# Kernel tuning notes

Measured on AMD Instinct MI355X. Metric: run time of the kernel, lower is better.

Reference implementation:

```python
import jax, jax.numpy as jnp
import numpy as np

DIM = 256
QK_DIM = 256
NUM_HEADS = 8
N_WIN = 7
TOPK = 4
SCALE = QK_DIM ** (-0.5)


def setup_inputs() -> dict:
    key = jax.random.key(0)
    k1, k2, k3 = jax.random.split(key, 3)
    N, D, H, W, C = 2, 8, 56, 56, DIM
    x = jax.random.normal(k1, (N, D, H, W, C), dtype=jnp.float32)
    # QKVLinear: Linear(dim, qk_dim + qk_dim + dim)
    Wqkv = jax.random.normal(k2, (C, 2 * QK_DIM + DIM), dtype=jnp.float32) * 0.02
    bqkv = jnp.zeros((2 * QK_DIM + DIM,), dtype=jnp.float32)
    Wo = jax.random.normal(k3, (DIM, DIM), dtype=jnp.float32) * 0.02
    bo = jnp.zeros((DIM,), dtype=jnp.float32)
    return {"x": x, "Wqkv": Wqkv, "bqkv": bqkv, "Wo": Wo, "bo": bo}


def reference(x, Wqkv, bqkv, Wo, bo):
    N, D, H, W, C = x.shape
    j = i = N_WIN
    h, w = H // j, W // i
    p2, w2 = j * i, h * w
    n = N * D
    m = NUM_HEADS
    ch = QK_DIM // m   # qk head dim
    cv = DIM // m      # v head dim

    # n t (j h) (i w) c -> n t (j i) h w c
    xw = x.reshape(N, D, j, h, i, w, C).transpose(0, 1, 2, 4, 3, 5, 6)
    xw = xw.reshape(N, D, p2, h, w, C)

    # QKVLinear then split into q / kv
    qkv = xw @ Wqkv + bqkv                       # (N,D,p2,h,w,2qk+dim)
    q = qkv[..., :QK_DIM]                        # (N,D,p2,h,w,qk)
    kv = qkv[..., QK_DIM:]                       # (N,D,p2,h,w,qk+dim)

    # inter-frame shift: frame t uses kv of frame t+1; last frame keeps its own
    kv = jnp.concatenate([kv[:, 1:], kv[:, -1:]], axis=1)

    q = q.reshape(n, p2, h, w, QK_DIM)
    kv = kv.reshape(n, p2, h, w, QK_DIM + DIM)
    q_pix = q.reshape(n, p2, w2, QK_DIM)
    kv_pix = kv.reshape(n, p2, w2, QK_DIM + DIM)  # identity kv_down

    # window-level routing (diff_routing=False -> detached)
    q_win = jax.lax.stop_gradient(q.mean(axis=(2, 3)))                  # (n,p2,qk)
    k_win = jax.lax.stop_gradient(kv[..., :QK_DIM].mean(axis=(2, 3)))   # (n,p2,qk)
    attn_logit = jnp.einsum('npc,nqc->npq', q_win * SCALE, k_win)       # (n,p2,p2)
    topk_logit, r_idx = jax.lax.top_k(attn_logit, TOPK)                 # (n,p2,topk)
    r_weight = jax.nn.softmax(topk_logit, axis=-1)  # computed, unused (mul_weight='none')

    # gather kv of routed windows: (n,p2,topk,w2,qk+dim)
    kv_sel = jax.vmap(lambda kvp, idx: kvp[idx])(kv_pix, r_idx)

    k_sel = kv_sel[..., :QK_DIM].reshape(n, p2, TOPK * w2, m, ch)
    v_sel = kv_sel[..., QK_DIM:].reshape(n, p2, TOPK * w2, m, cv)
    qh = q_pix.reshape(n, p2, w2, m, ch)

    attn = jnp.einsum('npqmc,npkmc->npmqk', qh * SCALE, k_sel)  # (n,p2,m,w2,topk*w2)
    attn = jax.nn.softmax(attn, axis=-1)
    out = jnp.einsum('npmqk,npkmc->npqmc', attn, v_sel).reshape(n, p2, w2, C)

    # (n j i) (h w) c -> N D (j h) (i w) c
    out = out.reshape(N, D, j, i, h, w, C).transpose(0, 1, 2, 4, 3, 5, 6)
    out = out.reshape(N, D, H, W, C)
    out = out @ Wo + bo
    return out
```

## Files before the change

### kernel.cpp

```cpp
#include <hip/hip_runtime.h>
#include <hip/hip_bf16.h>
#include <math.h>

#define QSC 0.09016844f

typedef __attribute__((ext_vector_type(8))) short bf16x8;
typedef __attribute__((ext_vector_type(4))) float f32x4;

__device__ __forceinline__ ushort f2bf(float f) {
    unsigned u = __float_as_uint(f);
    return (ushort)((u + 0x7FFFu + ((u >> 16) & 1u)) >> 16);
}

__device__ __forceinline__ unsigned pk2bf(float a, float b) {
    __hip_bfloat162 h = __float22bfloat162_rn(make_float2(a, b));
    return *(unsigned*)&h;
}

__device__ __forceinline__ void gl_lds16(const ushort* g, ushort* l) {
    __builtin_amdgcn_global_load_lds(
        (const __attribute__((address_space(1))) unsigned int*)g,
        (__attribute__((address_space(3))) unsigned int*)l, 16, 0, 0);
}

__device__ __forceinline__ int swz(int row) { return (row ^ (row >> 2)) & 3; }

__device__ __forceinline__ int token_to_xrow(int t) {
    int nd  = t / 3136;
    int r   = t % 3136;
    int p   = r >> 6;
    int pix = r & 63;
    int j = p / 7, i = p % 7;
    int hh = pix >> 3, ww = pix & 7;
    return nd * 3136 + (j * 8 + hh) * 56 + (i * 8 + ww);
}

__global__ __launch_bounds__(256) void k_prep(const float* __restrict__ x,
                                              const float* __restrict__ Wqkv,
                                              const float* __restrict__ Wo,
                                              ushort* __restrict__ xg,
                                              float* __restrict__ xmean,
                                              ushort* __restrict__ Wqkvt,
                                              ushort* __restrict__ Wot) {
    int b = blockIdx.x;
    int tid = threadIdx.x;
    if (b >= 784) {
        int bb = b - 784;
        if (bb < 768) Wqkvt[bb * 256 + tid] = f2bf(Wqkv[(size_t)tid * 768 + bb]);
        else { int n = bb - 768; Wot[n * 256 + tid] = f2bf(Wo[(size_t)tid * 256 + n]); }
        return;
    }
    int nd = b / 49, p = b % 49;
    int j = p / 7, i = p % 7;
    const float* xb = x + ((size_t)nd * 3136 + (j * 8) * 56 + i * 8) * 256 + tid;
    ushort* xo = xg + (size_t)b * 64 * 256 + tid;
    float s = 0.f;
#pragma unroll 2
    for (int hh = 0; hh < 8; ++hh)
#pragma unroll
        for (int ww = 0; ww < 8; ++ww) {
            float v = xb[(size_t)(hh * 56 + ww) * 256];
            s += v;
            xo[(size_t)(hh * 8 + ww) * 256] = f2bf(v);
        }
    xmean[(size_t)b * 256 + tid] = s * (1.f / 64.f);
}

__global__ __launch_bounds__(256) void k_winproj(const float* __restrict__ xmean,
                                                 const float* __restrict__ Wqkv,
                                                 const float* __restrict__ bqkv,
                                                 float* __restrict__ qwin,
                                                 float* __restrict__ kwin) {
    __shared__ float As[16 * 68];
    __shared__ float Bs[16 * 64];
    const int tid = threadIdx.x;
    const int m0 = blockIdx.y * 64;
    const int n0 = blockIdx.x * 64;

    const int ar = tid >> 2;
    const int ak = (tid & 3) * 4;
    const int arow = (m0 + ar < 784) ? (m0 + ar) : 783;
    const float* aptr = xmean + (size_t)arow * 256 + ak;

    const int bk = tid >> 4;
    const int bn = (tid & 15) * 4;
    const float* bptr = Wqkv + (size_t)bk * 768 + n0 + bn;

    const int ty = tid >> 4, tx = tid & 15;
    float acc[4][4] = {};

    for (int kt = 0; kt < 256; kt += 16) {
        float4 av = *(const float4*)(aptr + kt);
        float4 bv = *(const float4*)(bptr + (size_t)kt * 768);
        __syncthreads();
        As[(ak + 0) * 68 + ar] = av.x;
        As[(ak + 1) * 68 + ar] = av.y;
        As[(ak + 2) * 68 + ar] = av.z;
        As[(ak + 3) * 68 + ar] = av.w;
        *(float4*)&Bs[bk * 64 + bn] = bv;
        __syncthreads();
#pragma unroll
        for (int kk = 0; kk < 16; ++kk) {
            float4 a4 = *(const float4*)&As[kk * 68 + ty * 4];
            float4 b4 = *(const float4*)&Bs[kk * 64 + tx * 4];
            float a[4] = {a4.x, a4.y, a4.z, a4.w};
            float b[4] = {b4.x, b4.y, b4.z, b4.w};
#pragma unroll
            for (int ii = 0; ii < 4; ++ii)
#pragma unroll
                for (int jj = 0; jj < 4; ++jj) acc[ii][jj] += a[ii] * b[jj];
        }
    }
#pragma unroll
    for (int ii = 0; ii < 4; ++ii) {
        int t = m0 + ty * 4 + ii;
        if (t >= 784) continue;
#pragma unroll
        for (int jj = 0; jj < 4; ++jj) {
            int col = n0 + tx * 4 + jj;
            float v = acc[ii][jj] + bqkv[col];
            if (col < 256) qwin[(size_t)t * 256 + col] = v;
            else           kwin[(size_t)t * 256 + (col - 256)] = v;
        }
    }
}

__global__ __launch_bounds__(64) void k_route(const float* __restrict__ qwin,
                                              const float* __restrict__ kwin,
                                              int* __restrict__ ridx) {
    const int b = blockIdx.x;
    const int nd = b / 49;
    const int ndkv = ((nd & 7) == 7) ? nd : nd + 1;
    const int t = threadIdx.x;
    __shared__ float qs[256];
    for (int i = t; i < 256; i += 64) qs[i] = qwin[b * 256 + i];
    __syncthreads();
    float logit = -INFINITY;
    if (t < 49) {
        const float* kr = kwin + ((size_t)ndkv * 49 + t) * 256;
        float s = 0.f;
        for (int c = 0; c < 256; ++c) s += qs[c] * kr[c];
        logit = s;
    }
    for (int sel = 0; sel < 4; ++sel) {
        float v = logit;
        int ix = t;
        for (int off = 32; off > 0; off >>= 1) {
            float ov = __shfl_xor(v, off);
            int   oi = __shfl_xor(ix, off);
            if (ov > v || (ov == v && oi < ix)) { v = ov; ix = oi; }
        }
        if (t == 0) ridx[b * 4 + sel] = ix;
        if (t == ix) logit = -INFINITY;
    }
}

__global__ __launch_bounds__(256) void k_gemm_qkv(const ushort* __restrict__ A,
                                                  const ushort* __restrict__ Bt,
                                                  const float* __restrict__ bqkv,
                                                  ushort* __restrict__ q,
                                                  ushort* __restrict__ kv) {
    __shared__ ushort As[128 * 32];
    __shared__ ushort Bs[128 * 32];
    const int tid = threadIdx.x;
    const int wv = tid >> 6, ln = tid & 63;
    const int lane15 = ln & 15, quad = ln >> 4;
    const int m0 = blockIdx.y * 128, n0 = blockIdx.x * 128;
    const int row0 = tid >> 2, ck0 = tid & 3;

    const ushort* gA[2]; const ushort* gB[2];
    ushort* lA[2]; ushort* lB[2];
#pragma unroll
    for (int p = 0; p < 2; ++p) {
        int r = p * 64 + row0;
        int cks = ck0 ^ swz(r);
        gA[p] = A  + (size_t)(m0 + r) * 256 + cks * 8;
        gB[p] = Bt + (size_t)(n0 + r) * 256 + cks * 8;
        lA[p] = &As[(p * 256 + tid) * 8];
        lB[p] = &Bs[(p * 256 + tid) * 8];
    }

    f32x4 acc[4][4];
#pragma unroll
    for (int i = 0; i < 4; ++i)
#pragma unroll
        for (int j = 0; j < 4; ++j) acc[i][j] = (f32x4){0.f, 0.f, 0.f, 0.f};

    const int mb = (wv >> 1) * 64, nb = (wv & 1) * 64;

    for (int kt = 0; kt < 8; ++kt) {
        __syncthreads();
#pragma unroll
        for (int p = 0; p < 2; ++p) {
            gl_lds16(gA[p] + kt * 32, lA[p]);
            gl_lds16(gB[p] + kt * 32, lB[p]);
        }
        __syncthreads();
        bf16x8 aF[4], bF[4];
#pragma unroll
        for (int mt = 0; mt < 4; ++mt) {
            int r = mb + mt * 16 + lane15;
            aF[mt] = *(const bf16x8*)&As[r * 32 + (quad ^ swz(r)) * 8];
        }
#pragma unroll
        for (int nt = 0; nt < 4; ++nt) {
            int r = nb + nt * 16 + lane15;
            bF[nt] = *(const bf16x8*)&Bs[r * 32 + (quad ^ swz(r)) * 8];
        }
#pragma unroll
        for (int mt = 0; mt < 4; ++mt)
#pragma unroll
            for (int nt = 0; nt < 4; ++nt)
                acc[mt][nt] = __builtin_amdgcn_mfma_f32_16x16x32_bf16(aF[mt], bF[nt], acc[mt][nt], 0, 0, 0);
    }

#pragma unroll
    for (int mt = 0; mt < 4; ++mt) {
#pragma unroll
        for (int nt = 0; nt < 4; ++nt) {
            int col = n0 + nb + nt * 16 + lane15;
            float bias = bqkv[col];
#pragma unroll
            for (int r = 0; r < 4; ++r) {
                int t = m0 + mb + mt * 16 + quad * 4 + r;
                float v = acc[mt][nt][r] + bias;
                if (col < 256) q[(size_t)t * 256 + col] = f2bf(v * QSC);
                else           kv[(size_t)t * 512 + (col - 256)] = f2bf(v);
            }
        }
    }
}

__global__ __launch_bounds__(256) void k_gemm_o(const ushort* __restrict__ A,
                                                const ushort* __restrict__ Bt,
                                                const float* __restrict__ bo,
                                                float* __restrict__ out) {
    __shared__ ushort As[128 * 32];
    __shared__ ushort Bs[128 * 32];
    const int tid = threadIdx.x;
    const int wv = tid >> 6, ln = tid & 63;
    const int lane15 = ln & 15, quad = ln >> 4;
    const int m0 = blockIdx.y * 128, n0 = blockIdx.x * 128;
    const int row0 = tid >> 2, ck0 = tid & 3;

    const ushort* gA[2]; const ushort* gB[2];
    ushort* lA[2]; ushort* lB[2];
#pragma unroll
    for (int p = 0; p < 2; ++p) {
        int r = p * 64 + row0;
        int cks = ck0 ^ swz(r);
        gA[p] = A  + (size_t)(m0 + r) * 256 + cks * 8;
        gB[p] = Bt + (size_t)(n0 + r) * 256 + cks * 8;
        lA[p] = &As[(p * 256 + tid) * 8];
        lB[p] = &Bs[(p * 256 + tid) * 8];
    }

    f32x4 acc[4][4];
#pragma unroll
    for (int i = 0; i < 4; ++i)
#pragma unroll
        for (int j = 0; j < 4; ++j) acc[i][j] = (f32x4){0.f, 0.f, 0.f, 0.f};

    const int mb = (wv >> 1) * 64, nb = (wv & 1) * 64;

    for (int kt = 0; kt < 8; ++kt) {
        __syncthreads();
#pragma unroll
        for (int p = 0; p < 2; ++p) {
            gl_lds16(gA[p] + kt * 32, lA[p]);
            gl_lds16(gB[p] + kt * 32, lB[p]);
        }
        __syncthreads();
        bf16x8 aF[4], bF[4];
#pragma unroll
        for (int mt = 0; mt < 4; ++mt) {
            int r = mb + mt * 16 + lane15;
            aF[mt] = *(const bf16x8*)&As[r * 32 + (quad ^ swz(r)) * 8];
        }
#pragma unroll
        for (int nt = 0; nt < 4; ++nt) {
            int r = nb + nt * 16 + lane15;
            bF[nt] = *(const bf16x8*)&Bs[r * 32 + (quad ^ swz(r)) * 8];
        }
#pragma unroll
        for (int mt = 0; mt < 4; ++mt)
#pragma unroll
            for (int nt = 0; nt < 4; ++nt)
                acc[mt][nt] = __builtin_amdgcn_mfma_f32_16x16x32_bf16(aF[mt], bF[nt], acc[mt][nt], 0, 0, 0);
    }

#pragma unroll
    for (int mt = 0; mt < 4; ++mt) {
#pragma unroll
        for (int nt = 0; nt < 4; ++nt) {
            int col = n0 + nb + nt * 16 + lane15;
            float bias = bo[col];
#pragma unroll
            for (int r = 0; r < 4; ++r) {
                int t = m0 + mb + mt * 16 + quad * 4 + r;
                int xr = token_to_xrow(t);
                out[(size_t)xr * 256 + col] = acc[mt][nt][r] + bias;
            }
        }
    }
}

__global__ __launch_bounds__(256, 3) void k_attn(ushort* qbuf,
                                                 const ushort* __restrict__ kvbuf,
                                                 const int* __restrict__ ridx) {
    const int h = blockIdx.x, p = blockIdx.y, nd = blockIdx.z;
    const int ndkv = ((nd & 7) == 7) ? nd : nd + 1;
    const int tid = threadIdx.x;
    const int wv = tid >> 6, ln = tid & 63;
    const int lane15 = ln & 15, quad = ln >> 4;

    __shared__ ushort Ks[256 * 40];
    __shared__ ushort Vt[32 * 264];
    __shared__ ushort Ps[64 * 72];

    const int rb = (nd * 49 + p) * 4;
    int wid[4];
#pragma unroll
    for (int i = 0; i < 4; ++i) wid[i] = ridx[rb + i];

    const size_t kvband = (size_t)ndkv * 49;

    {
        int pix = tid >> 2, ck = tid & 3;
#pragma unroll
        for (int i = 0; i < 4; ++i) {
            size_t trow = (kvband + wid[i]) * 64 + pix;
            bf16x8 v = *(const bf16x8*)(kvbuf + trow * 512 + h * 32 + ck * 8);
            *(bf16x8*)&Ks[(i * 64 + pix) * 40 + ck * 8] = v;
        }
    }
    {
        int key_l = (tid & 31) * 2;
        int ch0 = (tid >> 5) * 4;
#pragma unroll
        for (int i = 0; i < 4; ++i) {
            size_t trow = (kvband + wid[i]) * 64;
            const ushort* g0 = kvbuf + (trow + key_l) * 512 + 256 + h * 32 + ch0;
            const ushort* g1 = g0 + 512;
            ushort4 a = *(const ushort4*)g0;
            ushort4 b = *(const ushort4*)g1;
            int kg = i * 64 + key_l;
            *(unsigned*)&Vt[(ch0 + 0) * 264 + kg] = (unsigned)a.x | ((unsigned)b.x << 16);
            *(unsigned*)&Vt[(ch0 + 1) * 264 + kg] = (unsigned)a.y | ((unsigned)b.y << 16);
            *(unsigned*)&Vt[(ch0 + 2) * 264 + kg] = (unsigned)a.z | ((unsigned)b.z << 16);
            *(unsigned*)&Vt[(ch0 + 3) * 264 + kg] = (unsigned)a.w | ((unsigned)b.w << 16);
        }
    }

    const size_t qrow0 = (size_t)(nd * 49 + p) * 64;
    bf16x8 bQ = *(const bf16x8*)(qbuf + (qrow0 + wv * 16 + lane15) * 256 + h * 32 + quad * 8);

    __syncthreads();

    f32x4 st[16];
#pragma unroll
    for (int t = 0; t < 16; ++t) {
        bf16x8 aK = *(const bf16x8*)&Ks[(t * 16 + lane15) * 40 + quad * 8];
        st[t] = __builtin_amdgcn_mfma_f32_16x16x32_bf16(aK, bQ, (f32x4){0.f, 0.f, 0.f, 0.f}, 0, 0, 0);
    }

    float sum = 0.f;
#pragma unroll
    for (int t = 0; t < 16; ++t)
#pragma unroll
        for (int r = 0; r < 4; ++r) {
            float e = __builtin_amdgcn_exp2f(st[t][r]);
            st[t][r] = e;
            sum += e;
        }
    sum += __shfl_xor(sum, 16);
    sum += __shfl_xor(sum, 32);
    const float inv = 1.f / sum;

    f32x4 oacc[2] = {{0.f, 0.f, 0.f, 0.f}, {0.f, 0.f, 0.f, 0.f}};
    const int prow = (wv * 16 + lane15) * 72;
#pragma unroll
    for (int cc = 0; cc < 4; ++cc) {
#pragma unroll
        for (int tt = 0; tt < 4; ++tt) {
            int t = cc * 4 + tt;
            uint2 pk;
            pk.x = pk2bf(st[t][0], st[t][1]);
            pk.y = pk2bf(st[t][2], st[t][3]);
            *(uint2*)&Ps[prow + tt * 16 + quad * 4] = pk;
        }
#pragma unroll
        for (int kt = 0; kt < 2; ++kt) {
            bf16x8 aP = *(const bf16x8*)&Ps[prow + kt * 32 + quad * 8];
#pragma unroll
            for (int nt = 0; nt < 2; ++nt) {
                bf16x8 bV = *(const bf16x8*)&Vt[(nt * 16 + lane15) * 264 + cc * 64 + kt * 32 + quad * 8];
                oacc[nt] = __builtin_amdgcn_mfma_f32_16x16x32_bf16(aP, bV, oacc[nt], 0, 0, 0);
            }
        }
    }

#pragma unroll
    for (int nt = 0; nt < 2; ++nt)
#pragma unroll
        for (int r = 0; r < 4; ++r) {
            int row = wv * 16 + quad * 4 + r;
            qbuf[(qrow0 + row) * 256 + h * 32 + nt * 16 + lane15] = f2bf(oacc[nt][r] * inv);
        }
}

extern "C" void kernel_launch(void* const* d_in, const int* in_sizes, int n_in,
                              void* d_out, int out_size, void* d_ws, size_t ws_size,
                              hipStream_t stream) {
    const float* x    = (const float*)d_in[0];
    const float* Wqkv = (const float*)d_in[1];
    const float* bqkv = (const float*)d_in[2];
    const float* Wo   = (const float*)d_in[3];
    const float* bo   = (const float*)d_in[4];
    float* out = (float*)d_out;

    char* ws = (char*)d_ws;
    ushort* xg    = (ushort*)ws;                    ws += (size_t)50176 * 256 * 2;
    ushort* q     = (ushort*)ws;                    ws += (size_t)50176 * 256 * 2;
    ushort* kv    = (ushort*)ws;                    ws += (size_t)50176 * 512 * 2;
    ushort* Wqkvt = (ushort*)ws;                    ws += (size_t)768 * 256 * 2;
    ushort* Wot   = (ushort*)ws;                    ws += (size_t)256 * 256 * 2;
    float*  xmean = (float*)ws;                     ws += (size_t)784 * 256 * 4;
    float*  qwin  = (float*)ws;                     ws += (size_t)784 * 256 * 4;
    float*  kwin  = (float*)ws;                     ws += (size_t)784 * 256 * 4;
    int*    ridx  = (int*)ws;

    k_prep    <<<1808, 256, 0, stream>>>(x, Wqkv, Wo, xg, xmean, Wqkvt, Wot);
    k_winproj <<<dim3(8, 13), 256, 0, stream>>>(xmean, Wqkv, bqkv, qwin, kwin);
    k_route   <<<784, 64, 0, stream>>>(qwin, kwin, ridx);
    k_gemm_qkv<<<dim3(6, 392), 256, 0, stream>>>(xg, Wqkvt, bqkv, q, kv);
    k_attn    <<<dim3(8, 49, 16), 256, 0, stream>>>(q, kv, ridx);
    k_gemm_o  <<<dim3(2, 392), 256, 0, stream>>>(q, Wot, bo, out);
}
```

Measured before the change: 248.9 us.

## Double-buffer GEMM LDS loads, remap blocks for XCD locality, parallelize routing

Both bf16 GEMM kernels now use double-buffered LDS tiles, prefetching the next K slice while MFMAs run on the current one. This replaces the two barriers per iteration with a single wait and barrier. The GEMM and attention kernels also remap block indices so consecutive work lands on the same XCD (lin&7 striping), aiming for better L2 reuse. The routing kernel splits each dot product across four waves with float4 loads. The costs are double the LDS per GEMM block, which may lower occupancy, and more index arithmetic.

```diff
diff --git a/kernel.cpp b/kernel.cpp
--- a/kernel.cpp
+++ b/kernel.cpp
@@ -125,33 +125,44 @@
     }
 }
 
-__global__ __launch_bounds__(64) void k_route(const float* __restrict__ qwin,
-                                              const float* __restrict__ kwin,
-                                              int* __restrict__ ridx) {
+__global__ __launch_bounds__(256) void k_route(const float* __restrict__ qwin,
+                                               const float* __restrict__ kwin,
+                                               int* __restrict__ ridx) {
     const int b = blockIdx.x;
     const int nd = b / 49;
     const int ndkv = ((nd & 7) == 7) ? nd : nd + 1;
-    const int t = threadIdx.x;
+    const int tid = threadIdx.x;
+    const int t = tid & 63, w = tid >> 6;
     __shared__ float qs[256];
-    for (int i = t; i < 256; i += 64) qs[i] = qwin[b * 256 + i];
+    __shared__ float part[4][64];
+    qs[tid] = qwin[b * 256 + tid];
     __syncthreads();
-    float logit = -INFINITY;
+    float s = 0.f;
     if (t < 49) {
-        const float* kr = kwin + ((size_t)ndkv * 49 + t) * 256;
-        float s = 0.f;
-        for (int c = 0; c < 256; ++c) s += qs[c] * kr[c];
-        logit = s;
-    }
-    for (int sel = 0; sel < 4; ++sel) {
-        float v = logit;
-        int ix = t;
-        for (int off = 32; off > 0; off >>= 1) {
-            float ov = __shfl_xor(v, off);
-            int   oi = __shfl_xor(ix, off);
-            if (ov > v || (ov == v && oi < ix)) { v = ov; ix = oi; }
-        }
-        if (t == 0) ridx[b * 4 + sel] = ix;
-        if (t == ix) logit = -INFINITY;
+        const float* kr = kwin + ((size_t)ndkv * 49 + t) * 256 + w * 64;
+#pragma unroll
+        for (int c = 0; c < 64; c += 4) {
+            float4 k4 = *(const float4*)(kr + c);
+            float4 q4 = *(const float4*)&qs[w * 64 + c];
+            s += q4.x * k4.x + q4.y * k4.y + q4.z * k4.z + q4.w * k4.w;
+        }
+    }
+    part[w][t] = s;
+    __syncthreads();
+    if (tid < 64) {
+        float logit = (t < 49) ? (part[0][t] + part[1][t] + part[2][t] + part[3][t])
+                               : -INFINITY;
+        for (int sel = 0; sel < 4; ++sel) {
+            float v = logit;
+            int ix = t;
+            for (int off = 32; off > 0; off >>= 1) {
+                float ov = __shfl_xor(v, off);
+                int   oi = __shfl_xor(ix, off);
+                if (ov > v || (ov == v && oi < ix)) { v = ov; ix = oi; }
+            }
+            if (t == 0) ridx[b * 4 + sel] = ix;
+            if (t == ix) logit = -INFINITY;
+        }
     }
 }
 
@@ -160,24 +171,27 @@
                                                   const float* __restrict__ bqkv,
                                                   ushort* __restrict__ q,
                                                   ushort* __restrict__ kv) {
-    __shared__ ushort As[128 * 32];
-    __shared__ ushort Bs[128 * 32];
+    __shared__ ushort As[2][128 * 32];
+    __shared__ ushort Bs[2][128 * 32];
     const int tid = threadIdx.x;
     const int wv = tid >> 6, ln = tid & 63;
     const int lane15 = ln & 15, quad = ln >> 4;
-    const int m0 = blockIdx.y * 128, n0 = blockIdx.x * 128;
+
+    const int lin  = blockIdx.x + blockIdx.y * 6;
+    const int work = (lin & 7) * 294 + (lin >> 3);
+    const int n0 = (work % 6) * 128;
+    const int m0 = (work / 6) * 128;
+
     const int row0 = tid >> 2, ck0 = tid & 3;
-
     const ushort* gA[2]; const ushort* gB[2];
-    ushort* lA[2]; ushort* lB[2];
+    int lofs[2];
 #pragma unroll
     for (int p = 0; p < 2; ++p) {
         int r = p * 64 + row0;
         int cks = ck0 ^ swz(r);
         gA[p] = A  + (size_t)(m0 + r) * 256 + cks * 8;
         gB[p] = Bt + (size_t)(n0 + r) * 256 + cks * 8;
-        lA[p] = &As[(p * 256 + tid) * 8];
-        lB[p] = &Bs[(p * 256 + tid) * 8];
+        lofs[p] = (p * 256 + tid) * 8;
     }
 
     f32x4 acc[4][4];
@@ -188,30 +202,45 @@
 
     const int mb = (wv >> 1) * 64, nb = (wv & 1) * 64;
 
+#pragma unroll
+    for (int p = 0; p < 2; ++p) {
+        gl_lds16(gA[p], &As[0][lofs[p]]);
+        gl_lds16(gB[p], &Bs[0][lofs[p]]);
+    }
+    asm volatile("s_waitcnt vmcnt(0)" ::: "memory");
+    __builtin_amdgcn_s_barrier();
+
+    int cur = 0;
+#pragma unroll
     for (int kt = 0; kt < 8; ++kt) {
-        __syncthreads();
-#pragma unroll
-        for (int p = 0; p < 2; ++p) {
-            gl_lds16(gA[p] + kt * 32, lA[p]);
-            gl_lds16(gB[p] + kt * 32, lB[p]);
-        }
-        __syncthreads();
+        if (kt < 7) {
+#pragma unroll
+            for (int p = 0; p < 2; ++p) {
+                gl_lds16(gA[p] + (kt + 1) * 32, &As[cur ^ 1][lofs[p]]);
+                gl_lds16(gB[p] + (kt + 1) * 32, &Bs[cur ^ 1][lofs[p]]);
+            }
+        }
+        __builtin_amdgcn_sched_barrier(0);
         bf16x8 aF[4], bF[4];
 #pragma unroll
         for (int mt = 0; mt < 4; ++mt) {
             int r = mb + mt * 16 + lane15;
-            aF[mt] = *(const bf16x8*)&As[r * 32 + (quad ^ swz(r)) * 8];
+            aF[mt] = *(const bf16x8*)&As[cur][r * 32 + (quad ^ swz(r)) * 8];
         }
 #pragma unroll
         for (int nt = 0; nt < 4; ++nt) {
             int r = nb + nt * 16 + lane15;
-            bF[nt] = *(const bf16x8*)&Bs[r * 32 + (quad ^ swz(r)) * 8];
+            bF[nt] = *(const bf16x8*)&Bs[cur][r * 32 + (quad ^ swz(r)) * 8];
         }
 #pragma unroll
         for (int mt = 0; mt < 4; ++mt)
 #pragma unroll
             for (int nt = 0; nt < 4; ++nt)
                 acc[mt][nt] = __builtin_amdgcn_mfma_f32_16x16x32_bf16(aF[mt], bF[nt], acc[mt][nt], 0, 0, 0);
+        __builtin_amdgcn_sched_barrier(0);
+        asm volatile("s_waitcnt vmcnt(0)" ::: "memory");
+        __builtin_amdgcn_s_barrier();
+        cur ^= 1;
     }
 
 #pragma unroll
@@ -235,24 +264,27 @@
                                                 const ushort* __restrict__ Bt,
                                                 const float* __restrict__ bo,
                                                 float* __restrict__ out) {
-    __shared__ ushort As[128 * 32];
-    __shared__ ushort Bs[128 * 32];
+    __shared__ ushort As[2][128 * 32];
+    __shared__ ushort Bs[2][128 * 32];
     const int tid = threadIdx.x;
     const int wv = tid >> 6, ln = tid & 63;
     const int lane15 = ln & 15, quad = ln >> 4;
-    const int m0 = blockIdx.y * 128, n0 = blockIdx.x * 128;
+
+    const int lin  = blockIdx.x + blockIdx.y * 2;
+    const int work = (lin & 7) * 98 + (lin >> 3);
+    const int n0 = (work % 2) * 128;
+    const int m0 = (work / 2) * 128;
+
     const int row0 = tid >> 2, ck0 = tid & 3;
-
     const ushort* gA[2]; const ushort* gB[2];
-    ushort* lA[2]; ushort* lB[2];
+    int lofs[2];
 #pragma unroll
     for (int p = 0; p < 2; ++p) {
         int r = p * 64 + row0;
         int cks = ck0 ^ swz(r);
         gA[p] = A  + (size_t)(m0 + r) * 256 + cks * 8;
         gB[p] = Bt + (size_t)(n0 + r) * 256 + cks * 8;
-        lA[p] = &As[(p * 256 + tid) * 8];
-        lB[p] = &Bs[(p * 256 + tid) * 8];
+        lofs[p] = (p * 256 + tid) * 8;
     }
 
     f32x4 acc[4][4];
@@ -263,30 +295,45 @@
 
     const int mb = (wv >> 1) * 64, nb = (wv & 1) * 64;
 
+#pragma unroll
+    for (int p = 0; p < 2; ++p) {
+        gl_lds16(gA[p], &As[0][lofs[p]]);
+        gl_lds16(gB[p], &Bs[0][lofs[p]]);
+    }
+    asm volatile("s_waitcnt vmcnt(0)" ::: "memory");
+    __builtin_amdgcn_s_barrier();
+
+    int cur = 0;
+#pragma unroll
     for (int kt = 0; kt < 8; ++kt) {
-        __syncthreads();
-#pragma unroll
-        for (int p = 0; p < 2; ++p) {
-            gl_lds16(gA[p] + kt * 32, lA[p]);
-            gl_lds16(gB[p] + kt * 32, lB[p]);
-        }
-        __syncthreads();
+        if (kt < 7) {
+#pragma unroll
+            for (int p = 0; p < 2; ++p) {
+                gl_lds16(gA[p] + (kt + 1) * 32, &As[cur ^ 1][lofs[p]]);
+                gl_lds16(gB[p] + (kt + 1) * 32, &Bs[cur ^ 1][lofs[p]]);
+            }
+        }
+        __builtin_amdgcn_sched_barrier(0);
         bf16x8 aF[4], bF[4];
 #pragma unroll
         for (int mt = 0; mt < 4; ++mt) {
             int r = mb + mt * 16 + lane15;
-            aF[mt] = *(const bf16x8*)&As[r * 32 + (quad ^ swz(r)) * 8];
+            aF[mt] = *(const bf16x8*)&As[cur][r * 32 + (quad ^ swz(r)) * 8];
         }
 #pragma unroll
         for (int nt = 0; nt < 4; ++nt) {
             int r = nb + nt * 16 + lane15;
-            bF[nt] = *(const bf16x8*)&Bs[r * 32 + (quad ^ swz(r)) * 8];
+            bF[nt] = *(const bf16x8*)&Bs[cur][r * 32 + (quad ^ swz(r)) * 8];
         }
 #pragma unroll
         for (int mt = 0; mt < 4; ++mt)
 #pragma unroll
             for (int nt = 0; nt < 4; ++nt)
                 acc[mt][nt] = __builtin_amdgcn_mfma_f32_16x16x32_bf16(aF[mt], bF[nt], acc[mt][nt], 0, 0, 0);
+        __builtin_amdgcn_sched_barrier(0);
+        asm volatile("s_waitcnt vmcnt(0)" ::: "memory");
+        __builtin_amdgcn_s_barrier();
+        cur ^= 1;
     }
 
 #pragma unroll
@@ -308,7 +355,13 @@
 __global__ __launch_bounds__(256, 3) void k_attn(ushort* qbuf,
                                                  const ushort* __restrict__ kvbuf,
                                                  const int* __restrict__ ridx) {
-    const int h = blockIdx.x, p = blockIdx.y, nd = blockIdx.z;
+    const int lin  = blockIdx.x + (blockIdx.y + blockIdx.z * 49) * 8;
+    const int work = (lin & 7) * 784 + (lin >> 3);
+    const int h = work & 7;
+    const int rest = work >> 3;
+    const int p = rest % 49;
+    const int nd = rest / 49;
+
     const int ndkv = ((nd & 7) == 7) ? nd : nd + 1;
     const int tid = threadIdx.x;
     const int wv = tid >> 6, ln = tid & 63;
@@ -432,7 +485,7 @@
 
     k_prep    <<<1808, 256, 0, stream>>>(x, Wqkv, Wo, xg, xmean, Wqkvt, Wot);
     k_winproj <<<dim3(8, 13), 256, 0, stream>>>(xmean, Wqkv, bqkv, qwin, kwin);
-    k_route   <<<784, 64, 0, stream>>>(qwin, kwin, ridx);
+    k_route   <<<784, 256, 0, stream>>>(qwin, kwin, ridx);
     k_gemm_qkv<<<dim3(6, 392), 256, 0, stream>>>(xg, Wqkvt, bqkv, q, kv);
     k_attn    <<<dim3(8, 49, 16), 256, 0, stream>>>(q, kv, ridx);
     k_gemm_o  <<<dim3(2, 392), 256, 0, stream>>>(q, Wot, bo, out);
```

Measured after the change: 233.4 us. -6.2%, faster.
